# Performance work log

Hardware: AMD Instinct MI355X
Metric: run time of the kernel (lower is better)

## Reference

```python
import jax, jax.numpy as jnp
import numpy as np

MIN_NORM = 1e-5
EPS = 1e-7
N_NODES = 100000
N_EDGES = 20000
NNZ = 640000
F_DIM = 128  # in_channels == out_channels
NUM_LAYERS = 2
MAX_NORM = 1e6


def _cosh(x):
    return jnp.cosh(jnp.clip(x, -15.0, 15.0))


def _sinh(x):
    return jnp.sinh(jnp.clip(x, -15.0, 15.0))


def _arcosh(x):
    # caller already clamps x >= 1 + eps
    return jnp.log(x + jnp.sqrt(jnp.clip(x * x - 1.0, EPS)))


def proj(x, c):
    K = 1.0 / c
    y = x[:, 1:]
    y_sq = jnp.sum(y * y, axis=1, keepdims=True)
    x0 = jnp.sqrt(jnp.clip(K + y_sq, EPS))
    return jnp.concatenate([x0, y], axis=1)


def proj_tan0(u):
    # zero out the time-like (first) coordinate
    return jnp.concatenate([jnp.zeros_like(u[:, :1]), u[:, 1:]], axis=1)


def expmap0(u, c):
    K = 1.0 / c
    sqrtK = jnp.sqrt(K)
    x = u[:, 1:]
    x_norm = jnp.clip(jnp.linalg.norm(x, axis=1, keepdims=True), MIN_NORM)
    theta = x_norm / sqrtK
    res0 = sqrtK * _cosh(theta)
    res_rest = sqrtK * _sinh(theta) * x / x_norm
    return proj(jnp.concatenate([res0, res_rest], axis=1), c)


def logmap0(x, c):
    K = 1.0 / c
    sqrtK = jnp.sqrt(K)
    y = x[:, 1:]
    y_norm = jnp.clip(jnp.linalg.norm(y, axis=1, keepdims=True), MIN_NORM)
    theta = jnp.clip(x[:, 0:1] / sqrtK, 1.0 + EPS)
    rest = sqrtK * _arcosh(theta) * y / y_norm
    return jnp.concatenate([jnp.zeros_like(x[:, :1]), rest], axis=1)


def minkowski_norm(u):
    dot = jnp.sum(u * u, axis=-1, keepdims=True) - 2.0 * (u[:, 0:1] * u[:, 0:1])
    return jnp.sqrt(jnp.clip(dot, EPS))


def proj_tan(u, x):
    ux = jnp.sum(x[:, 1:] * u[:, 1:], axis=1, keepdims=True)
    v0 = ux / jnp.clip(x[:, 0:1], EPS)
    return jnp.concatenate([v0, u[:, 1:]], axis=1)


def expmap(u, x, c):
    K = 1.0 / c
    sqrtK = jnp.sqrt(K)
    normu = jnp.clip(minkowski_norm(u), None, MAX_NORM)
    theta = jnp.clip(normu / sqrtK, MIN_NORM)
    result = _cosh(theta) * x + _sinh(theta) * u / theta
    return proj(result, c)


def ptransp0(x, u, c):
    K = 1.0 / c
    sqrtK = jnp.sqrt(K)
    x0 = x[:, 0:1]
    y = x[:, 1:]
    y_norm = jnp.clip(jnp.linalg.norm(y, axis=1, keepdims=True), MIN_NORM)
    y_hat = y / y_norm
    v = jnp.concatenate([-y_norm, (sqrtK - x0) * y_hat], axis=1)
    alpha = jnp.sum(y_hat * u[:, 1:], axis=1, keepdims=True) / sqrtK
    res = u - alpha * v
    return proj_tan(res, x)


def mobius_add(x, y, c):
    u = logmap0(y, c)
    v = ptransp0(x, u, c)
    return expmap(v, x, c)


def hyp_block(x, node_idx, edge_idx, bias, c_in, c_out):
    # tangent features at origin
    x = proj_tan0(logmap0(x, c_in))
    # degree normalizations (hyperedge_weight = ones, EW_weight = None)
    ones_nnz = jnp.ones((node_idx.shape[0],), dtype=x.dtype)
    D = jax.ops.segment_sum(ones_nnz, node_idx, num_segments=N_NODES)
    D = jnp.where(D > 0, 1.0 / D, 0.0)
    B = jax.ops.segment_sum(ones_nnz, edge_idx, num_segments=N_EDGES)
    B = jnp.where(B > 0, 1.0 / B, 0.0)
    # propagate nodes -> hyperedges (norm = B at destination edge)
    m1 = B[edge_idx][:, None] * x[node_idx]            # [nnz, F]
    e_feat = jax.ops.segment_sum(m1, edge_idx, num_segments=N_EDGES)
    # propagate hyperedges -> nodes (norm = D at destination node)
    m2 = D[node_idx][:, None] * e_feat[edge_idx]       # [nnz, F]
    out = jax.ops.segment_sum(m2, node_idx, num_segments=N_NODES)
    # hyperbolic bias add + activation
    bias_t = proj_tan0(bias[None, :])
    hyp_bias = proj(expmap0(bias_t, c_in), c_in)
    res = proj(out, c_in)
    res = proj(mobius_add(res, hyp_bias, c_in), c_in)
    out = jax.nn.leaky_relu(logmap0(res, c_in), 0.01)
    out = proj_tan0(out)
    return proj(expmap0(out, c_out), c_out)


def reference(x, hyperedge_index, curvatures, biases):
    node_idx = hyperedge_index[0]
    edge_idx = hyperedge_index[1]
    # encoder: prepend zero time coordinate, lift to hyperboloid
    h = jnp.concatenate([jnp.zeros_like(x[:, :1]), x], axis=1)
    c0 = jax.nn.softplus(curvatures[0])
    h = proj(expmap0(proj_tan0(h), c0), c0)
    for i in range(NUM_LAYERS):
        c_in = jax.nn.softplus(curvatures[i])
        c_out = jax.nn.softplus(curvatures[i + 1])
        h = hyp_block(h, node_idx, edge_idx, biases[i], c_in, c_out)
    # decoder
    c_last = jax.nn.softplus(curvatures[-1])
    return proj_tan0(logmap0(h, c_last))


def setup_inputs() -> dict:
    key = jax.random.key(0)
    k1, k2, k3, k4 = jax.random.split(key, 4)
    x = jax.random.normal(k1, (N_NODES, F_DIM - 1), dtype=jnp.float32)
    node_idx = jax.random.randint(k2, (NNZ,), 0, N_NODES)
    edge_idx = jax.random.randint(k3, (NNZ,), 0, N_EDGES)
    edge_idx = edge_idx.at[-1].set(N_EDGES - 1)  # ensure max edge id = E-1
    hyperedge_index = jnp.stack([node_idx, edge_idx], axis=0).astype(jnp.int64)
    curvatures = jnp.full((NUM_LAYERS + 1,), 0.1, dtype=jnp.float32)
    biases = 0.02 * jax.random.normal(k4, (NUM_LAYERS, F_DIM), dtype=jnp.float32)
    return {"x": x, "hyperedge_index": hyperedge_index, "curvatures": curvatures, "biases": biases}
```

## Files before the change

kernel.cpp:

```cpp
#include <hip/hip_runtime.h>
#include <hip/hip_fp16.h>
#include <math.h>

#define N_NODESc 100000
#define N_EDGESc 20000
#define NNZc     640000
#define FD       128
#define WE       96
#define WN       48
#define NBKT     256
#define EPB      2048
#define NCHUNKS  313
#define ESHIFT   7
#define NSHIFT   9
#define NBKT_E   157
#define NBKT_N   196
#define STAGEBLK 6250
#define MIN_NORMf 1e-5f
#define EPSf      1e-7f
#define MAX_NORMf 1e6f

__device__ __forceinline__ float wred(float v){
  #pragma unroll
  for(int m=32;m;m>>=1) v += __shfl_xor(v, m, 64);
  return v;
}
__device__ __forceinline__ void wred2_16(float& a, float& b){
  #pragma unroll
  for(int m=8;m;m>>=1){
    float ta = __shfl_xor(a, m, 64);
    float tb = __shfl_xor(b, m, 64);
    a += ta; b += tb;
  }
}

__device__ __forceinline__ void h8_acc(const float4 h, float4& a0, float4& a1){
  const __half2* hp = (const __half2*)&h;
  float2 f0 = __half22float2(hp[0]);
  float2 f1 = __half22float2(hp[1]);
  float2 f2 = __half22float2(hp[2]);
  float2 f3 = __half22float2(hp[3]);
  a0.x += f0.x; a0.y += f0.y; a0.z += f1.x; a0.w += f1.y;
  a1.x += f2.x; a1.y += f2.y; a1.z += f3.x; a1.w += f3.y;
}
__device__ __forceinline__ float4 pack_h8(const float4 a, const float4 b){
  float4 out;
  __half2* hp = (__half2*)&out;
  hp[0] = __float22half2_rn(make_float2(a.x,a.y));
  hp[1] = __float22half2_rn(make_float2(a.z,a.w));
  hp[2] = __float22half2_rn(make_float2(b.x,b.y));
  hp[3] = __float22half2_rn(make_float2(b.z,b.w));
  return out;
}

__device__ __forceinline__ void get_pair(const int* hei, int k, int f64, int& n, int& e){
  if(f64){ n = hei[2*k]; e = hei[2*NNZc + 2*k]; }
  else   { n = hei[k];   e = hei[NNZc + k]; }
}

__global__ void k_prep(const int* hei, const float* curv, const float* biases,
                       int* flag, float* scal, float* ubias, int* gHist, int* gCur){
  int tid = threadIdx.x;
  gHist[tid] = 0;  gHist[tid + NBKT] = 0;
  gCur[tid]  = 0;  gCur[tid + NBKT]  = 0;
  if(tid < 64){
    int lane = tid;
    int hi = hei[2*lane+1];
    unsigned long long b = __ballot(hi != 0);
    if(lane==0) flag[0] = (b==0ull) ? 1 : 0;
    if(lane==0){
      scal[0] = log1pf(expf(curv[0]));
      scal[1] = log1pf(expf(curv[1]));
      scal[2] = log1pf(expf(curv[2]));
    }
    int d0 = 2*lane, d1 = d0+1;
    for(int L=0; L<2; ++L){
      float u0 = (d0==0) ? 0.f : biases[L*FD + d0];
      float u1 = biases[L*FD + d1];
      ubias[L*FD + d0] = u0;
      ubias[L*FD + d1] = u1;
      float uu = wred(u0*u0 + u1*u1);
      if(lane==0) scal[3+L] = uu;
    }
  }
}

__global__ void k_stage_hist(const float* x, float4* xh,
                             const int* hei, const int* flag, int* gHist){
  int bid = blockIdx.x;
  if(bid < STAGEBLK){
    int t = bid*256 + threadIdx.x;
    int node = t >> 4, l16 = t & 15;
    int d8 = 8*l16;
    const float* r = x + (size_t)node*(FD-1);
    float4 p0, p1;
    if(l16==0){
      float4 q0 = *(const float4*)(r);
      p1 = *(const float4*)(r + 3);
      p0 = make_float4(0.f, q0.x, q0.y, q0.z);
    } else {
      p0 = *(const float4*)(r + d8 - 1);
      p1 = *(const float4*)(r + d8 + 3);
    }
    xh[(size_t)node*16 + l16] = pack_h8(p0, p1);
  } else {
    __shared__ int h[NBKT];
    int tid = threadIdx.x;
    int hb = bid - STAGEBLK;
    int side = hb & 1;
    int chunk = hb >> 1;
    h[tid] = 0; __syncthreads();
    int f64 = flag[0];
    int base = chunk*EPB;
    #pragma unroll
    for(int j=0;j<8;++j){
      int k = base + j*256 + tid;
      if(k < NNZc){
        int n,e; get_pair(hei,k,f64,n,e);
        int b = side ? (n>>NSHIFT) : (e>>ESHIFT);
        atomicAdd(&h[b],1);
      }
    }
    __syncthreads();
    int c = h[tid];
    if(c>0) atomicAdd(&gHist[side*NBKT+tid], c);
  }
}

__global__ void k_part(const int* hei, const int* flag, const int* gHist, int* gCur,
                       unsigned long long* partE, unsigned long long* partN){
  __shared__ int sscan[NBKT];
  __shared__ int h[NBKT];
  __shared__ int bbase[NBKT];
  int tid = threadIdx.x;
  int side = blockIdx.x & 1;
  int chunk = blockIdx.x >> 1;

  int hv = gHist[side*NBKT+tid];
  sscan[tid] = hv;
  h[tid] = 0;
  __syncthreads();
  for(int off=1; off<NBKT; off<<=1){
    int t2 = (tid>=off)? sscan[tid-off] : 0;
    __syncthreads();
    sscan[tid] += t2;
    __syncthreads();
  }
  int sbase = sscan[tid] - hv;

  int f64 = flag[0];
  int base = chunk*EPB;
  int keyv[8], payl[8], rank[8], bkt[8];
  #pragma unroll
  for(int j=0;j<8;++j){
    int k = base + j*256 + tid;
    if(k < NNZc){
      int n,e; get_pair(hei,k,f64,n,e);
      if(side==0){ keyv[j]=e; payl[j]=n; bkt[j]=e>>ESHIFT; }
      else       { keyv[j]=n; payl[j]=e; bkt[j]=n>>NSHIFT; }
      rank[j] = atomicAdd(&h[bkt[j]],1);
    } else bkt[j] = -1;
  }
  __syncthreads();
  int c = h[tid];
  if(c>0) bbase[tid] = sbase + atomicAdd(&gCur[side*NBKT+tid], c);
  __syncthreads();
  unsigned long long* part = side ? partN : partE;
  #pragma unroll
  for(int j=0;j<8;++j){
    if(bkt[j]>=0){
      int pos = bbase[bkt[j]] + rank[j];
      part[pos] = ((unsigned long long)(unsigned)keyv[j]<<32) | (unsigned)payl[j];
    }
  }
}

__global__ void k_build(const unsigned long long* partE, const unsigned long long* partN,
                        const int* gHist, int* curE, int* curN, int* eEll, int* nEll){
  __shared__ int sscan[NBKT];
  __shared__ int lcur[512];
  int bid = blockIdx.x;
  int side = (bid >= NBKT_E) ? 1 : 0;
  int bkt  = side ? bid - NBKT_E : bid;
  int tid = threadIdx.x;

  int hv = gHist[side*NBKT+tid];
  sscan[tid] = hv; __syncthreads();
  for(int off=1; off<NBKT; off<<=1){
    int t2 = (tid>=off)? sscan[tid-off] : 0;
    __syncthreads();
    sscan[tid] += t2;
    __syncthreads();
  }
  int cntB  = gHist[side*NBKT+bkt];
  int start = sscan[bkt] - cntB;

  int nkeys = side ? 512 : 128;
  for(int i=tid; i<nkeys; i+=256) lcur[i] = 0;
  __syncthreads();

  const unsigned long long* part = side ? partN : partE;
  int* ell = side ? nEll : eEll;
  int W = side ? WN : WE;
  int keybase = side ? (bkt<<NSHIFT) : (bkt<<ESHIFT);
  for(int i=tid; i<cntB; i+=256){
    unsigned long long v = part[start+i];
    int key = (int)(v>>32);
    int pay = (int)(unsigned)v;
    int pos = atomicAdd(&lcur[key-keybase], 1);
    if(pos<W) ell[(size_t)key*W+pos] = pay;
  }
  __syncthreads();

  int total = side ? N_NODESc : N_EDGESc;
  int* cur  = side ? curN : curE;
  for(int i=tid; i<nkeys; i+=256){
    int key = keybase + i;
    if(key < total) cur[key] = lcur[i];
  }
}

__global__ void k_edge_gather(const int* curE, const int* eEll, const float4* rowsH, float4* efeatH){
  int t = blockIdx.x*blockDim.x + threadIdx.x;
  int w    = t >> 6;
  int lane = t & 63;
  int quad = lane >> 4, l16 = lane & 15;
  int edge = w*2 + (quad>>1);
  int qh   = quad & 1;

  int cnt = curE[edge];
  int use = cnt<WE ? cnt : WE;
  const int* ent = eEll + (size_t)edge*WE;

  float4 aA = make_float4(0.f,0.f,0.f,0.f);
  float4 aB = make_float4(0.f,0.f,0.f,0.f);
  int j = qh;
  for(; j+14 < use; j += 16){
    int r0 = ent[j];    int r1 = ent[j+2];
    int r2 = ent[j+4];  int r3 = ent[j+6];
    int r4 = ent[j+8];  int r5 = ent[j+10];
    int r6 = ent[j+12]; int r7 = ent[j+14];
    float4 h0 = rowsH[(size_t)r0*16 + l16];
    float4 h1 = rowsH[(size_t)r1*16 + l16];
    float4 h2 = rowsH[(size_t)r2*16 + l16];
    float4 h3 = rowsH[(size_t)r3*16 + l16];
    float4 h4 = rowsH[(size_t)r4*16 + l16];
    float4 h5 = rowsH[(size_t)r5*16 + l16];
    float4 h6 = rowsH[(size_t)r6*16 + l16];
    float4 h7 = rowsH[(size_t)r7*16 + l16];
    h8_acc(h0,aA,aB); h8_acc(h1,aA,aB); h8_acc(h2,aA,aB); h8_acc(h3,aA,aB);
    h8_acc(h4,aA,aB); h8_acc(h5,aA,aB); h8_acc(h6,aA,aB); h8_acc(h7,aA,aB);
  }
  for(; j < use; j += 2){
    float4 h = rowsH[(size_t)ent[j]*16 + l16];
    h8_acc(h,aA,aB);
  }
  aA.x += __shfl_xor(aA.x, 16, 64); aA.y += __shfl_xor(aA.y, 16, 64);
  aA.z += __shfl_xor(aA.z, 16, 64); aA.w += __shfl_xor(aA.w, 16, 64);
  aB.x += __shfl_xor(aB.x, 16, 64); aB.y += __shfl_xor(aB.y, 16, 64);
  aB.z += __shfl_xor(aB.z, 16, 64); aB.w += __shfl_xor(aB.w, 16, 64);

  if(qh==0){
    float b = cnt>0 ? __fdividef(1.f,(float)cnt) : 0.f;
    aA.x*=b; aA.y*=b; aA.z*=b; aA.w*=b;
    aB.x*=b; aB.y*=b; aB.z*=b; aB.w*=b;
    efeatH[(size_t)edge*16 + l16] = pack_h8(aA, aB);
  }
}

template<int OUTH>
__global__ void k_node_epilogue(const int* curN, const int* nEll, const float4* efeatH,
                                const float* scal, const float* ubias, int layer,
                                float4* outH, float* outF){
  int t = blockIdx.x*blockDim.x + threadIdx.x;
  int w    = t >> 6;
  int lane = t & 63;
  if(w >= N_NODESc/4) return;
  int quad = lane >> 4, l16 = lane & 15;
  int node = w*4 + quad;
  int d8 = 8*l16;

  float cin = scal[layer];
  float K   = __fdividef(1.f, cin);
  float sK  = sqrtf(K);
  float isK = __fdividef(1.f, sK);
  float uu  = scal[3+layer];

  int cnt = curN[node];
  float dv = cnt>0 ? __fdividef(1.f,(float)cnt) : 0.f;
  int use = cnt<WN ? cnt : WN;
  const int* ent = nEll + (size_t)node*WN;

  float4 aA = make_float4(0.f,0.f,0.f,0.f);
  float4 aB = make_float4(0.f,0.f,0.f,0.f);
  int j = 0;
  for(; j+3 < use; j += 4){
    int r0 = ent[j];   int r1 = ent[j+1];
    int r2 = ent[j+2]; int r3 = ent[j+3];
    float4 h0 = efeatH[(size_t)r0*16 + l16];
    float4 h1 = efeatH[(size_t)r1*16 + l16];
    float4 h2 = efeatH[(size_t)r2*16 + l16];
    float4 h3 = efeatH[(size_t)r3*16 + l16];
    h8_acc(h0,aA,aB); h8_acc(h1,aA,aB); h8_acc(h2,aA,aB); h8_acc(h3,aA,aB);
  }
  for(; j < use; ++j){
    float4 h = efeatH[(size_t)ent[j]*16 + l16];
    h8_acc(h,aA,aB);
  }
  aA.x*=dv; aA.y*=dv; aA.z*=dv; aA.w*=dv;
  aB.x*=dv; aB.y*=dv; aB.z*=dv; aB.w*=dv;

  const float4* up = (const float4*)(ubias + layer*FD + d8);
  float4 uA = up[0], uB = up[1];

  float ysq   = aA.x*aA.x + aA.y*aA.y + aA.z*aA.z + aA.w*aA.w
              + aB.x*aB.x + aB.y*aB.y + aB.z*aB.z + aB.w*aB.w;
  float dotAU = aA.x*uA.x + aA.y*uA.y + aA.z*uA.z + aA.w*uA.w
              + aB.x*uB.x + aB.y*uB.y + aB.z*uB.z + aB.w*uB.w;
  wred2_16(ysq, dotAU);

  float res0  = sqrtf(fmaxf(K + ysq, EPSf));
  float ynorm = fmaxf(sqrtf(ysq), MIN_NORMf);
  float iyn   = __fdividef(1.f, ynorm);

  float alpha = dotAU*iyn*isK;
  float ab    = alpha*(sK - res0);
  float abiyn = ab*iyn;
  float4 rA, rB;
  rA.x = fmaf(-abiyn, aA.x, uA.x); rA.y = fmaf(-abiyn, aA.y, uA.y);
  rA.z = fmaf(-abiyn, aA.z, uA.z); rA.w = fmaf(-abiyn, aA.w, uA.w);
  rB.x = fmaf(-abiyn, aB.x, uB.x); rB.y = fmaf(-abiyn, aB.y, uB.y);
  rB.z = fmaf(-abiyn, aB.z, uB.z); rB.w = fmaf(-abiyn, aB.w, uB.w);
  float ux  = fmaf(-ab, ynorm, dotAU);
  float v0s = ux * __fdividef(1.f, fmaxf(res0, EPSf));
  float rsq = fmaf(ab, ab, fmaf(-2.f*abiyn, dotAU, uu));

  float mink  = fmaxf(fmaf(-v0s, v0s, rsq), EPSf);
  float normu = fminf(sqrtf(mink), MAX_NORMf);
  float th    = fmaxf(normu*isK, MIN_NORMf);
  float thc   = fminf(th, 15.f);
  float e  = __expf(thc);
  float ei = __fdividef(1.f, e);
  float ch = 0.5f*(e + ei);
  float sh = 0.5f*(e - ei);
  float sth = sh*__fdividef(1.f, th);
  float4 qA, qB;
  qA.x = fmaf(ch, aA.x, sth*rA.x); qA.y = fmaf(ch, aA.y, sth*rA.y);
  qA.z = fmaf(ch, aA.z, sth*rA.z); qA.w = fmaf(ch, aA.w, sth*rA.w);
  qB.x = fmaf(ch, aB.x, sth*rB.x); qB.y = fmaf(ch, aB.y, sth*rB.y);
  qB.z = fmaf(ch, aB.z, sth*rB.z); qB.w = fmaf(ch, aB.w, sth*rB.w);

  float ysq2 = fmaxf(ch*ch*ysq + 2.f*ch*sth*ux + sth*sth*rsq, 0.f);
  float h0   = sqrtf(fmaxf(K + ysq2, EPSf));
  float yn3  = fmaxf(sqrtf(ysq2), MIN_NORMf);
  float th3  = fmaxf(h0*isK, 1.f+EPSf);
  float acs  = __logf(th3 + sqrtf(fmaxf(fmaf(th3,th3,-1.f), EPSf)));
  float fac  = sK*acs*__fdividef(1.f, yn3);
  float4 tA, tB;
  tA.x = fac*qA.x; tA.y = fac*qA.y; tA.z = fac*qA.z; tA.w = fac*qA.w;
  tB.x = fac*qB.x; tB.y = fac*qB.y; tB.z = fac*qB.z; tB.w = fac*qB.w;
  tA.x = tA.x>=0.f ? tA.x : 0.01f*tA.x;
  tA.y = tA.y>=0.f ? tA.y : 0.01f*tA.y;
  tA.z = tA.z>=0.f ? tA.z : 0.01f*tA.z;
  tA.w = tA.w>=0.f ? tA.w : 0.01f*tA.w;
  tB.x = tB.x>=0.f ? tB.x : 0.01f*tB.x;
  tB.y = tB.y>=0.f ? tB.y : 0.01f*tB.y;
  tB.z = tB.z>=0.f ? tB.z : 0.01f*tB.z;
  tB.w = tB.w>=0.f ? tB.w : 0.01f*tB.w;
  if(l16==0) tA.x = 0.f;

  if(OUTH){
    outH[(size_t)node*16 + l16] = pack_h8(tA, tB);
  } else {
    float4* op = (float4*)(outF + (size_t)node*FD + d8);
    op[0] = tA;
    op[1] = tB;
  }
}

extern "C" void kernel_launch(void* const* d_in, const int* in_sizes, int n_in,
                              void* d_out, int out_size, void* d_ws, size_t ws_size,
                              hipStream_t stream) {
  const float* x      = (const float*)d_in[0];
  const int*   hei    = (const int*)d_in[1];
  const float* curv   = (const float*)d_in[2];
  const float* biases = (const float*)d_in[3];
  float* out = (float*)d_out;

  char* p = (char*)d_ws;
  auto alloc = [&](size_t bytes){ char* r = p; p += (bytes + 255) & ~(size_t)255; return r; };
  int*   flag  = (int*)  alloc(4);
  float* scal  = (float*)alloc(16*4);
  float* ubias = (float*)alloc(2*FD*4);
  int*   gHist = (int*)  alloc(2*NBKT*4);
  int*   gCur  = (int*)  alloc(2*NBKT*4);
  int*   curE  = (int*)  alloc((size_t)N_EDGESc*4);
  int*   curN  = (int*)  alloc((size_t)N_NODESc*4);
  unsigned long long* partE = (unsigned long long*)alloc((size_t)NNZc*8);
  unsigned long long* partN = (unsigned long long*)alloc((size_t)NNZc*8);
  int*   eEll  = (int*)  alloc((size_t)N_EDGESc*WE*4);
  int*   nEll  = (int*)  alloc((size_t)N_NODESc*WN*4);
  float4* xh    = (float4*)alloc((size_t)N_NODESc*16*16);
  float4* tangH = (float4*)alloc((size_t)N_NODESc*16*16);
  float4* efeatH= (float4*)alloc((size_t)N_EDGESc*16*16);

  k_prep      <<<1, 256, 0, stream>>>(hei, curv, biases, flag, scal, ubias, gHist, gCur);
  k_stage_hist<<<STAGEBLK + 2*NCHUNKS, 256, 0, stream>>>(x, xh, hei, flag, gHist);
  k_part      <<<2*NCHUNKS, 256, 0, stream>>>(hei, flag, gHist, gCur, partE, partN);
  k_build     <<<NBKT_E + NBKT_N, 256, 0, stream>>>(partE, partN, gHist, curE, curN, eEll, nEll);

  k_edge_gather     <<<(N_EDGESc/2*64)/256, 256, 0, stream>>>(curE, eEll, xh, efeatH);
  k_node_epilogue<1><<<(N_NODESc/4*64)/256, 256, 0, stream>>>(curN, nEll, efeatH, scal, ubias, 0, tangH, out);
  k_edge_gather     <<<(N_EDGESc/2*64)/256, 256, 0, stream>>>(curE, eEll, tangH, efeatH);
  k_node_epilogue<0><<<(N_NODESc/4*64)/256, 256, 0, stream>>>(curN, nEll, efeatH, scal, ubias, 1, tangH, out);
}
```

Before: 179.9 us.

## Pack node/edge index pairs into 32-bit keys and unroll node gather by eight

The histogram pass now reads the index pairs with vector loads and writes a compact 32-bit packed (edge<<17 | node) array. The partition and build kernels then use that array instead of re-reading the raw (possibly int64) hyperedge_index, and move 32-bit keys instead of 64-bit ones. This halves the partition buffer traffic and removes repeated strided index reads. The node epilogue gather loop also gains an 8-wide unrolled path to put more loads in flight. The packing assumes node ids fit in 17 bits and edge ids in 15.

```diff
diff --git a/kernel.cpp b/kernel.cpp
--- a/kernel.cpp
+++ b/kernel.cpp
@@ -16,6 +16,7 @@
 #define NBKT_E   157
 #define NBKT_N   196
 #define STAGEBLK 6250
+#define NMASK    0x1FFFFu
 #define MIN_NORMf 1e-5f
 #define EPSf      1e-7f
 #define MAX_NORMf 1e6f
@@ -51,11 +52,6 @@
   hp[2] = __float22half2_rn(make_float2(b.x,b.y));
   hp[3] = __float22half2_rn(make_float2(b.z,b.w));
   return out;
-}
-
-__device__ __forceinline__ void get_pair(const int* hei, int k, int f64, int& n, int& e){
-  if(f64){ n = hei[2*k]; e = hei[2*NNZc + 2*k]; }
-  else   { n = hei[k];   e = hei[NNZc + k]; }
 }
 
 __global__ void k_prep(const int* hei, const float* curv, const float* biases,
@@ -86,7 +82,7 @@
 }
 
 __global__ void k_stage_hist(const float* x, float4* xh,
-                             const int* hei, const int* flag, int* gHist){
+                             const int* hei, const int* flag, int* gHist, unsigned* pk){
   int bid = blockIdx.x;
   if(bid < STAGEBLK){
     int t = bid*256 + threadIdx.x;
@@ -113,12 +109,29 @@
     int f64 = flag[0];
     int base = chunk*EPB;
     #pragma unroll
-    for(int j=0;j<8;++j){
-      int k = base + j*256 + tid;
+    for(int it=0; it<4; ++it){
+      int k = base + it*512 + tid*2;
       if(k < NNZc){
-        int n,e; get_pair(hei,k,f64,n,e);
-        int b = side ? (n>>NSHIFT) : (e>>ESHIFT);
-        atomicAdd(&h[b],1);
+        int n0,n1,e0,e1;
+        if(f64){
+          int4 aa = *(const int4*)(hei + 2*k);
+          int4 bb = *(const int4*)(hei + 2*NNZc + 2*k);
+          n0=aa.x; n1=aa.z; e0=bb.x; e1=bb.z;
+        } else {
+          int2 aa = *(const int2*)(hei + k);
+          int2 bb = *(const int2*)(hei + NNZc + k);
+          n0=aa.x; n1=aa.y; e0=bb.x; e1=bb.y;
+        }
+        if(side==0){
+          atomicAdd(&h[e0>>ESHIFT],1);
+          atomicAdd(&h[e1>>ESHIFT],1);
+          uint2 pv = make_uint2(((unsigned)e0<<17)|(unsigned)n0,
+                                ((unsigned)e1<<17)|(unsigned)n1);
+          *(uint2*)(pk + k) = pv;
+        } else {
+          atomicAdd(&h[n0>>NSHIFT],1);
+          atomicAdd(&h[n1>>NSHIFT],1);
+        }
       }
     }
     __syncthreads();
@@ -127,8 +140,8 @@
   }
 }
 
-__global__ void k_part(const int* hei, const int* flag, const int* gHist, int* gCur,
-                       unsigned long long* partE, unsigned long long* partN){
+__global__ void k_part(const unsigned* pk, const int* gHist, int* gCur,
+                       unsigned* partE, unsigned* partN){
   __shared__ int sscan[NBKT];
   __shared__ int h[NBKT];
   __shared__ int bbase[NBKT];
@@ -148,34 +161,38 @@
   }
   int sbase = sscan[tid] - hv;
 
-  int f64 = flag[0];
   int base = chunk*EPB;
-  int keyv[8], payl[8], rank[8], bkt[8];
+  unsigned kv[8]; int rank[8], bkt[8];
   #pragma unroll
-  for(int j=0;j<8;++j){
-    int k = base + j*256 + tid;
-    if(k < NNZc){
-      int n,e; get_pair(hei,k,f64,n,e);
-      if(side==0){ keyv[j]=e; payl[j]=n; bkt[j]=e>>ESHIFT; }
-      else       { keyv[j]=n; payl[j]=e; bkt[j]=n>>NSHIFT; }
-      rank[j] = atomicAdd(&h[bkt[j]],1);
-    } else bkt[j] = -1;
+  for(int it=0; it<2; ++it){
+    int k = base + it*1024 + tid*4;
+    bool ok = k < NNZc;
+    uint4 v = ok ? *(const uint4*)(pk + k) : make_uint4(0,0,0,0);
+    kv[it*4+0]=v.x; kv[it*4+1]=v.y; kv[it*4+2]=v.z; kv[it*4+3]=v.w;
+    #pragma unroll
+    for(int j=0;j<4;++j){
+      int idx = it*4+j;
+      if(ok){
+        bkt[idx] = side ? (int)((kv[idx]&NMASK)>>NSHIFT) : (int)(kv[idx]>>(17+ESHIFT));
+        rank[idx] = atomicAdd(&h[bkt[idx]],1);
+      } else bkt[idx] = -1;
+    }
   }
   __syncthreads();
   int c = h[tid];
   if(c>0) bbase[tid] = sbase + atomicAdd(&gCur[side*NBKT+tid], c);
   __syncthreads();
-  unsigned long long* part = side ? partN : partE;
+  unsigned* part = side ? partN : partE;
   #pragma unroll
   for(int j=0;j<8;++j){
     if(bkt[j]>=0){
       int pos = bbase[bkt[j]] + rank[j];
-      part[pos] = ((unsigned long long)(unsigned)keyv[j]<<32) | (unsigned)payl[j];
-    }
-  }
-}
-
-__global__ void k_build(const unsigned long long* partE, const unsigned long long* partN,
+      part[pos] = kv[j];
+    }
+  }
+}
+
+__global__ void k_build(const unsigned* partE, const unsigned* partN,
                         const int* gHist, int* curE, int* curN, int* eEll, int* nEll){
   __shared__ int sscan[NBKT];
   __shared__ int lcur[512];
@@ -199,14 +216,14 @@
   for(int i=tid; i<nkeys; i+=256) lcur[i] = 0;
   __syncthreads();
 
-  const unsigned long long* part = side ? partN : partE;
+  const unsigned* part = side ? partN : partE;
   int* ell = side ? nEll : eEll;
   int W = side ? WN : WE;
   int keybase = side ? (bkt<<NSHIFT) : (bkt<<ESHIFT);
   for(int i=tid; i<cntB; i+=256){
-    unsigned long long v = part[start+i];
-    int key = (int)(v>>32);
-    int pay = (int)(unsigned)v;
+    unsigned v = part[start+i];
+    int key = side ? (int)(v&NMASK) : (int)(v>>17);
+    int pay = side ? (int)(v>>17)   : (int)(v&NMASK);
     int pos = atomicAdd(&lcur[key-keybase], 1);
     if(pos<W) ell[(size_t)key*W+pos] = pay;
   }
@@ -294,6 +311,22 @@
   float4 aA = make_float4(0.f,0.f,0.f,0.f);
   float4 aB = make_float4(0.f,0.f,0.f,0.f);
   int j = 0;
+  for(; j+7 < use; j += 8){
+    int r0 = ent[j];   int r1 = ent[j+1];
+    int r2 = ent[j+2]; int r3 = ent[j+3];
+    int r4 = ent[j+4]; int r5 = ent[j+5];
+    int r6 = ent[j+6]; int r7 = ent[j+7];
+    float4 h0 = efeatH[(size_t)r0*16 + l16];
+    float4 h1 = efeatH[(size_t)r1*16 + l16];
+    float4 h2 = efeatH[(size_t)r2*16 + l16];
+    float4 h3 = efeatH[(size_t)r3*16 + l16];
+    float4 h4 = efeatH[(size_t)r4*16 + l16];
+    float4 h5 = efeatH[(size_t)r5*16 + l16];
+    float4 h6 = efeatH[(size_t)r6*16 + l16];
+    float4 h7 = efeatH[(size_t)r7*16 + l16];
+    h8_acc(h0,aA,aB); h8_acc(h1,aA,aB); h8_acc(h2,aA,aB); h8_acc(h3,aA,aB);
+    h8_acc(h4,aA,aB); h8_acc(h5,aA,aB); h8_acc(h6,aA,aB); h8_acc(h7,aA,aB);
+  }
   for(; j+3 < use; j += 4){
     int r0 = ent[j];   int r1 = ent[j+1];
     int r2 = ent[j+2]; int r3 = ent[j+3];
@@ -396,8 +429,9 @@
   int*   gCur  = (int*)  alloc(2*NBKT*4);
   int*   curE  = (int*)  alloc((size_t)N_EDGESc*4);
   int*   curN  = (int*)  alloc((size_t)N_NODESc*4);
-  unsigned long long* partE = (unsigned long long*)alloc((size_t)NNZc*8);
-  unsigned long long* partN = (unsigned long long*)alloc((size_t)NNZc*8);
+  unsigned* pk    = (unsigned*)alloc((size_t)NNZc*4);
+  unsigned* partE = (unsigned*)alloc((size_t)NNZc*4);
+  unsigned* partN = (unsigned*)alloc((size_t)NNZc*4);
   int*   eEll  = (int*)  alloc((size_t)N_EDGESc*WE*4);
   int*   nEll  = (int*)  alloc((size_t)N_NODESc*WN*4);
   float4* xh    = (float4*)alloc((size_t)N_NODESc*16*16);
@@ -405,8 +439,8 @@
   float4* efeatH= (float4*)alloc((size_t)N_EDGESc*16*16);
 
   k_prep      <<<1, 256, 0, stream>>>(hei, curv, biases, flag, scal, ubias, gHist, gCur);
-  k_stage_hist<<<STAGEBLK + 2*NCHUNKS, 256, 0, stream>>>(x, xh, hei, flag, gHist);
-  k_part      <<<2*NCHUNKS, 256, 0, stream>>>(hei, flag, gHist, gCur, partE, partN);
+  k_stage_hist<<<STAGEBLK + 2*NCHUNKS, 256, 0, stream>>>(x, xh, hei, flag, gHist, pk);
+  k_part      <<<2*NCHUNKS, 256, 0, stream>>>(pk, gHist, gCur, partE, partN);
   k_build     <<<NBKT_E + NBKT_N, 256, 0, stream>>>(partE, partN, gHist, curE, curN, eEll, nEll);
 
   k_edge_gather     <<<(N_EDGESc/2*64)/256, 256, 0, stream>>>(curE, eEll, xh, efeatH);
```

After: 186.5 us. 1.04x slower.
